# Optimization experiments

Hardware: AMD Instinct MI355X
Metric: run time of the kernel (lower is better)

The kernel has to match this reference:

```python
import jax, jax.numpy as jnp
import numpy as np

N = 100000
E = 1600000
IN_CH, HID_CH, OUT_CH = 128, 64, 32


def setup_inputs() -> dict:
    key = jax.random.key(0)
    ks = jax.random.split(key, 6)
    x = jax.random.normal(ks[0], (N, IN_CH), dtype=jnp.float32)
    ei = jax.random.randint(ks[1], (2, E), 0, N, dtype=jnp.int64)
    W1 = jax.random.normal(ks[2], (IN_CH, HID_CH), dtype=jnp.float32) * 0.05
    b1 = jax.random.normal(ks[3], (HID_CH,), dtype=jnp.float32) * 0.05
    W2 = jax.random.normal(ks[4], (HID_CH, OUT_CH), dtype=jnp.float32) * 0.05
    b2 = jax.random.normal(ks[5], (OUT_CH,), dtype=jnp.float32) * 0.05
    return {"x": x, "ei": ei, "W1": W1, "b1": b1, "W2": W2, "b2": b2}


def gcn_layer(x, sa, da, n):
    # degree with self-loops already appended in sa/da
    deg = jax.ops.segment_sum(jnp.ones((sa.shape[0],), x.dtype), da, num_segments=n)
    prod = deg[sa] * deg[da]
    norm = jnp.where(prod > 0, jax.lax.rsqrt(prod), 0.0)  # (deg_s*deg_d)^-0.5, inf->0
    msg = x[sa] * norm[:, None]            # [E+N, C] gather + scale
    return jax.ops.segment_sum(msg, da, num_segments=n)  # scatter_add


def reference(x, ei, W1, b1, W2, b2):
    n = x.shape[0]
    loop = jnp.arange(n, dtype=ei.dtype)
    sa = jnp.concatenate([ei[0], loop])
    da = jnp.concatenate([ei[1], loop])
    h = gcn_layer(x @ W1 + b1, sa, da, n)
    h = jax.nn.relu(h)
    # dropout: eval mode (training=False) -> identity
    return gcn_layer(h @ W2 + b2, sa, da, n)
```

## Files before the change

### kernel.cpp

```cpp
#include <hip/hip_runtime.h>

#define NN 100000
#define NE 1600000
#define IN_CH 128
#define HID_CH 64
#define OUT_CH 32
#define NBUCK 391
#define CHUNKA 8192

typedef unsigned short ushort_t;
typedef _Float16 half2_t __attribute__((ext_vector_type(2)));

__device__ inline ushort_t f2bf(float f) {
    union { float f; unsigned u; } v; v.f = f;
    unsigned r = v.u + 0x7fff + ((v.u >> 16) & 1);
    return (ushort_t)(r >> 16);
}
__device__ inline float blo(unsigned u) {
    union { unsigned x; float f; } v; v.x = u << 16; return v.f;
}
__device__ inline float bhi(unsigned u) {
    union { unsigned x; float f; } v; v.x = u & 0xffff0000u; return v.f;
}
__device__ inline unsigned pkh(float a, float b) {
    union { half2_t h; unsigned u; } v;
    v.h[0] = (_Float16)a; v.h[1] = (_Float16)b;
    return v.u;
}
__device__ inline half2_t u2h(unsigned u) {
    union { unsigned u; half2_t h; } v; v.u = u; return v.h;
}
__device__ inline float fdot2(unsigned a, unsigned b, float c) {
#if __has_builtin(__builtin_amdgcn_fdot2)
    return __builtin_amdgcn_fdot2(u2h(a), u2h(b), c, false);
#else
    half2_t ha = u2h(a), hb = u2h(b);
    return c + (float)ha[0] * (float)hb[0] + (float)ha[1] * (float)hb[1];
#endif
}

__global__ __launch_bounds__(256) void k_bhist(const int* __restrict__ da,
                                               int* __restrict__ bcnt) {
    __shared__ int hist[NBUCK];
    int t = threadIdx.x;
    for (int i = t; i < NBUCK; i += 256) hist[i] = 0;
    __syncthreads();
    int base = blockIdx.x * CHUNKA;
    for (int i = 0; i < CHUNKA; i += 256) {
        int e = base + i + t;
        if (e < NE) atomicAdd(&hist[da[e] >> 8], 1);
    }
    __syncthreads();
    for (int i = t; i < NBUCK; i += 256) {
        int c = hist[i];
        if (c) atomicAdd(&bcnt[i], c);
    }
}

__global__ __launch_bounds__(512) void k_bscan(const int* __restrict__ bcnt,
                                               int* __restrict__ bbase,
                                               int* __restrict__ bcur,
                                               int* __restrict__ rowptr) {
    __shared__ int lds[512];
    int t = threadIdx.x;
    int v = (t < NBUCK) ? bcnt[t] : 0;
    lds[t] = v;
    __syncthreads();
    for (int off = 1; off < 512; off <<= 1) {
        int x = (t >= off) ? lds[t - off] : 0;
        __syncthreads();
        lds[t] += x;
        __syncthreads();
    }
    int excl = lds[t] - v;
    if (t < NBUCK) { bbase[t] = excl; bcur[t] = excl; }
    if (t == 0) { bbase[NBUCK] = NE; rowptr[NN] = NE; }
}

__global__ __launch_bounds__(256) void k_bfill(const int* __restrict__ sa,
                                               const int* __restrict__ da,
                                               int* __restrict__ bcur,
                                               unsigned* __restrict__ ebuf) {
    __shared__ int hist[NBUCK];
    __shared__ int lcur[NBUCK];
    int t = threadIdx.x;
    for (int i = t; i < NBUCK; i += 256) hist[i] = 0;
    __syncthreads();
    int base = blockIdx.x * CHUNKA;
    for (int i = 0; i < CHUNKA; i += 256) {
        int e = base + i + t;
        if (e < NE) atomicAdd(&hist[da[e] >> 8], 1);
    }
    __syncthreads();
    for (int b = t; b < NBUCK; b += 256) {
        int c = hist[b];
        lcur[b] = c ? atomicAdd(&bcur[b], c) : 0;
    }
    __syncthreads();
    for (int i = 0; i < CHUNKA; i += 256) {
        int e = base + i + t;
        if (e < NE) {
            int d = da[e];
            int p = atomicAdd(&lcur[d >> 8], 1);
            ebuf[p] = ((unsigned)sa[e] << 8) | (unsigned)(d & 255);
        }
    }
}

__global__ __launch_bounds__(256) void k_bfine(const unsigned* __restrict__ ebuf,
                                               const int* __restrict__ bbase,
                                               int* __restrict__ rowptr,
                                               float* __restrict__ rs,
                                               int* __restrict__ col) {
    __shared__ int cnt[256];
    __shared__ int cur[256];
    __shared__ int scn[256];
    int b = blockIdx.x, t = threadIdx.x;
    int nb = NN - b * 256; if (nb > 256) nb = 256;
    int beg = bbase[b], end = bbase[b + 1];
    cnt[t] = 0;
    __syncthreads();
    for (int i = beg + t; i < end; i += 256) atomicAdd(&cnt[ebuf[i] & 255], 1);
    __syncthreads();
    int v = cnt[t];
    scn[t] = v;
    __syncthreads();
    for (int off = 1; off < 256; off <<= 1) {
        int x = (t >= off) ? scn[t - off] : 0;
        __syncthreads();
        scn[t] += x;
        __syncthreads();
    }
    int excl = scn[t] - v;
    if (t < nb) {
        rowptr[b * 256 + t] = beg + excl;
        rs[b * 256 + t] = rsqrtf((float)(v + 1));
        cur[t] = beg + excl;
    }
    __syncthreads();
    for (int i = beg + t; i < end; i += 256) {
        unsigned p = ebuf[i];
        int pos = atomicAdd(&cur[p & 255], 1);
        col[pos] = (int)(p >> 8);
    }
}

#define SWZU1(n, k2) ((n) * 64 + ((k2) ^ ((((n) & 7)) << 2)))
#define SWZ2(n, k) ((n) * 64 + ((k) ^ ((((n) & 7)) << 2)))

__global__ __launch_bounds__(256, 4) void k_gemm1(
    const float* __restrict__ x, const float* __restrict__ W1,
    const float* __restrict__ b1, const float* __restrict__ rs,
    ushort_t* __restrict__ xsb) {
    __shared__ unsigned xth[64 * 64];
    __shared__ unsigned w1h[64 * 64];
    int t = threadIdx.x;
    int base = blockIdx.x * 64;

#pragma unroll
    for (int i = 0; i < 8; ++i) {
        int flat = i * 1024 + t * 4;
        int node = flat >> 7, k0 = flat & 127;
        int gn = base + node;
        float4 v = make_float4(0.f, 0.f, 0.f, 0.f);
        if (gn < NN) v = *(const float4*)(x + (size_t)gn * IN_CH + k0);
        uint2 pk;
        pk.x = pkh(v.x, v.y);
        pk.y = pkh(v.z, v.w);
        *(uint2*)&xth[SWZU1(node, k0 >> 1)] = pk;
    }
#pragma unroll
    for (int i = 0; i < 16; ++i) {
        int idx = i * 256 + t;
        int k2 = idx >> 6, c = idx & 63;
        float f0 = W1[(2 * k2) * 64 + c];
        float f1 = W1[(2 * k2 + 1) * 64 + c];
        w1h[idx] = pkh(f0, f1);
    }
    __syncthreads();

    int tn = t & 15, tc = t >> 4;
    int c0 = tc * 4;
    float acc[4][4];
#pragma unroll
    for (int a = 0; a < 4; ++a)
#pragma unroll
        for (int b = 0; b < 4; ++b) acc[a][b] = 0.f;

    for (int k2 = 0; k2 < 64; k2 += 2) {
        uint2 xu[4];
#pragma unroll
        for (int jn = 0; jn < 4; ++jn)
            xu[jn] = *(uint2*)&xth[SWZU1(tn + jn * 16, k2)];
        uint4 w0 = *(uint4*)&w1h[(k2 + 0) * 64 + c0];
        uint4 w1 = *(uint4*)&w1h[(k2 + 1) * 64 + c0];
        unsigned wq0[4] = {w0.x, w0.y, w0.z, w0.w};
        unsigned wq1[4] = {w1.x, w1.y, w1.z, w1.w};
#pragma unroll
        for (int jn = 0; jn < 4; ++jn)
#pragma unroll
            for (int jc = 0; jc < 4; ++jc) {
                acc[jn][jc] = fdot2(xu[jn].x, wq0[jc], acc[jn][jc]);
                acc[jn][jc] = fdot2(xu[jn].y, wq1[jc], acc[jn][jc]);
            }
    }

    float4 bb = *(const float4*)&b1[c0];
#pragma unroll
    for (int jn = 0; jn < 4; ++jn) {
        int gn = base + tn + jn * 16;
        if (gn < NN) {
            float r = rs[gn];
            uint2 pk;
            pk.x = (unsigned)f2bf((acc[jn][0] + bb.x) * r) |
                   ((unsigned)f2bf((acc[jn][1] + bb.y) * r) << 16);
            pk.y = (unsigned)f2bf((acc[jn][2] + bb.z) * r) |
                   ((unsigned)f2bf((acc[jn][3] + bb.w) * r) << 16);
            *(uint2*)&xsb[(size_t)gn * HID_CH + c0] = pk;
        }
    }
}

__global__ __launch_bounds__(256) void k_agg1(
    const int* __restrict__ rowptr, const int* __restrict__ col,
    const ushort_t* __restrict__ xsb, const float* __restrict__ rs,
    ushort_t* __restrict__ hb) {
    int gid = blockIdx.x * blockDim.x + threadIdx.x;
    int n = gid >> 6;
    if (n >= NN) return;
    int lane = threadIdx.x & 63;
    int g = lane >> 4;
    unsigned c0 = (unsigned)(lane & 15) * 4;
    int beg = rowptr[n], end = rowptr[n + 1];

    float a0 = 0.f, a1 = 0.f, a2 = 0.f, a3 = 0.f;
    if (g == 0) {
        uint2 sv = *(const uint2*)&xsb[(unsigned)n * 64u + c0];
        a0 = blo(sv.x); a1 = bhi(sv.x); a2 = blo(sv.y); a3 = bhi(sv.y);
    }

    int i = beg;
    for (; i + 16 <= end; i += 16) {
        int s0 = col[i + g];
        int s1 = col[i + 4 + g];
        int s2 = col[i + 8 + g];
        int s3 = col[i + 12 + g];
        uint2 v0 = *(const uint2*)&xsb[(unsigned)s0 * 64u + c0];
        uint2 v1 = *(const uint2*)&xsb[(unsigned)s1 * 64u + c0];
        uint2 v2 = *(const uint2*)&xsb[(unsigned)s2 * 64u + c0];
        uint2 v3 = *(const uint2*)&xsb[(unsigned)s3 * 64u + c0];
        a0 += blo(v0.x); a1 += bhi(v0.x); a2 += blo(v0.y); a3 += bhi(v0.y);
        a0 += blo(v1.x); a1 += bhi(v1.x); a2 += blo(v1.y); a3 += bhi(v1.y);
        a0 += blo(v2.x); a1 += bhi(v2.x); a2 += blo(v2.y); a3 += bhi(v2.y);
        a0 += blo(v3.x); a1 += bhi(v3.x); a2 += blo(v3.y); a3 += bhi(v3.y);
    }
    for (; i + 4 <= end; i += 4) {
        int s0 = col[i + g];
        uint2 v0 = *(const uint2*)&xsb[(unsigned)s0 * 64u + c0];
        a0 += blo(v0.x); a1 += bhi(v0.x); a2 += blo(v0.y); a3 += bhi(v0.y);
    }
    int r = end - i;
    if (g < r) {
        int s0 = col[i + g];
        uint2 v0 = *(const uint2*)&xsb[(unsigned)s0 * 64u + c0];
        a0 += blo(v0.x); a1 += bhi(v0.x); a2 += blo(v0.y); a3 += bhi(v0.y);
    }

    a0 += __shfl_xor(a0, 16); a1 += __shfl_xor(a1, 16);
    a2 += __shfl_xor(a2, 16); a3 += __shfl_xor(a3, 16);
    a0 += __shfl_xor(a0, 32); a1 += __shfl_xor(a1, 32);
    a2 += __shfl_xor(a2, 32); a3 += __shfl_xor(a3, 32);

    if (g == 0) {
        float rn = rs[n];
        uint2 pk;
        pk.x = (unsigned)f2bf(fmaxf(a0 * rn, 0.f)) |
               ((unsigned)f2bf(fmaxf(a1 * rn, 0.f)) << 16);
        pk.y = (unsigned)f2bf(fmaxf(a2 * rn, 0.f)) |
               ((unsigned)f2bf(fmaxf(a3 * rn, 0.f)) << 16);
        *(uint2*)&hb[(unsigned)n * 64u + c0] = pk;
    }
}

__global__ __launch_bounds__(256) void k_gemm2(
    const ushort_t* __restrict__ hb, const float* __restrict__ W2,
    const float* __restrict__ b2, const float* __restrict__ rs,
    ushort_t* __restrict__ ysb) {
    __shared__ float ht[64 * 64];
    __shared__ float w2s[64 * 32];
    int t = threadIdx.x;
    int base = blockIdx.x * 64;

#pragma unroll
    for (int i = 0; i < 8; ++i) {
        int uidx = i * 256 + t;
        int node = uidx >> 5, k2 = uidx & 31;
        int gn = base + node;
        unsigned u = 0;
        if (gn < NN) u = *(const unsigned*)&hb[(size_t)gn * HID_CH + k2 * 2];
        float2 f; f.x = blo(u); f.y = bhi(u);
        *(float2*)&ht[SWZ2(node, k2 * 2)] = f;
    }
#pragma unroll
    for (int i = 0; i < 2; ++i) {
        int flat = i * 1024 + t * 4;
        *(float4*)&w2s[flat] = *(const float4*)(W2 + flat);
    }
    __syncthreads();

    int tn = t & 15, tc = t >> 4;
    int c0 = tc * 2;
    float acc[4][2];
#pragma unroll
    for (int a = 0; a < 4; ++a) { acc[a][0] = 0.f; acc[a][1] = 0.f; }

    for (int k0 = 0; k0 < 64; k0 += 4) {
        float xq[4][4], wq[4][2];
#pragma unroll
        for (int j = 0; j < 4; ++j)
            *(float2*)&wq[j][0] = *(float2*)&w2s[(k0 + j) * 32 + c0];
#pragma unroll
        for (int jn = 0; jn < 4; ++jn)
            *(float4*)&xq[jn][0] = *(float4*)&ht[SWZ2(tn + jn * 16, k0)];
#pragma unroll
        for (int jn = 0; jn < 4; ++jn)
#pragma unroll
            for (int j = 0; j < 4; ++j) {
                acc[jn][0] = fmaf(xq[jn][j], wq[j][0], acc[jn][0]);
                acc[jn][1] = fmaf(xq[jn][j], wq[j][1], acc[jn][1]);
            }
    }

    float2 bb = *(const float2*)&b2[c0];
#pragma unroll
    for (int jn = 0; jn < 4; ++jn) {
        int gn = base + tn + jn * 16;
        if (gn < NN) {
            float r = rs[gn];
            unsigned pk = (unsigned)f2bf((acc[jn][0] + bb.x) * r) |
                          ((unsigned)f2bf((acc[jn][1] + bb.y) * r) << 16);
            *(unsigned*)&ysb[(size_t)gn * OUT_CH + c0] = pk;
        }
    }
}

__global__ __launch_bounds__(256) void k_agg2(
    const int* __restrict__ rowptr, const int* __restrict__ col,
    const ushort_t* __restrict__ ysb, const float* __restrict__ rs,
    float* __restrict__ out) {
    int gid = blockIdx.x * blockDim.x + threadIdx.x;
    int n = gid >> 6;
    if (n >= NN) return;
    int lane = threadIdx.x & 63;
    int g = lane >> 3;
    unsigned c0 = (unsigned)(lane & 7) * 4;
    int beg = rowptr[n], end = rowptr[n + 1];

    float a0 = 0.f, a1 = 0.f, a2 = 0.f, a3 = 0.f;
    if (g == 0) {
        uint2 sv = *(const uint2*)&ysb[(unsigned)n * 32u + c0];
        a0 = blo(sv.x); a1 = bhi(sv.x); a2 = blo(sv.y); a3 = bhi(sv.y);
    }

    int i = beg;
    for (; i + 16 <= end; i += 16) {
        int s0 = col[i + g];
        int s1 = col[i + 8 + g];
        uint2 v0 = *(const uint2*)&ysb[(unsigned)s0 * 32u + c0];
        uint2 v1 = *(const uint2*)&ysb[(unsigned)s1 * 32u + c0];
        a0 += blo(v0.x); a1 += bhi(v0.x); a2 += blo(v0.y); a3 += bhi(v0.y);
        a0 += blo(v1.x); a1 += bhi(v1.x); a2 += blo(v1.y); a3 += bhi(v1.y);
    }
    if (i + 8 <= end) {
        int s0 = col[i + g];
        uint2 v0 = *(const uint2*)&ysb[(unsigned)s0 * 32u + c0];
        a0 += blo(v0.x); a1 += bhi(v0.x); a2 += blo(v0.y); a3 += bhi(v0.y);
        i += 8;
    }
    int r = end - i;
    if (g < r) {
        int s0 = col[i + g];
        uint2 v0 = *(const uint2*)&ysb[(unsigned)s0 * 32u + c0];
        a0 += blo(v0.x); a1 += bhi(v0.x); a2 += blo(v0.y); a3 += bhi(v0.y);
    }

    a0 += __shfl_xor(a0, 8);  a1 += __shfl_xor(a1, 8);
    a2 += __shfl_xor(a2, 8);  a3 += __shfl_xor(a3, 8);
    a0 += __shfl_xor(a0, 16); a1 += __shfl_xor(a1, 16);
    a2 += __shfl_xor(a2, 16); a3 += __shfl_xor(a3, 16);
    a0 += __shfl_xor(a0, 32); a1 += __shfl_xor(a1, 32);
    a2 += __shfl_xor(a2, 32); a3 += __shfl_xor(a3, 32);

    if (g == 0) {
        float rn = rs[n];
        float4 o;
        o.x = a0 * rn; o.y = a1 * rn; o.z = a2 * rn; o.w = a3 * rn;
        *(float4*)&out[(size_t)n * OUT_CH + c0] = o;
    }
}

extern "C" void kernel_launch(void* const* d_in, const int* in_sizes, int n_in,
                              void* d_out, int out_size, void* d_ws, size_t ws_size,
                              hipStream_t stream) {
    const float* x  = (const float*)d_in[0];
    const int*   ei = (const int*)d_in[1];
    const float* W1 = (const float*)d_in[2];
    const float* b1 = (const float*)d_in[3];
    const float* W2 = (const float*)d_in[4];
    const float* b2 = (const float*)d_in[5];
    const int* sa = ei;
    const int* da = ei + NE;

    char* ws = (char*)d_ws;
    size_t off = 0;
    auto alloc = [&](size_t bytes) {
        void* p = ws + off;
        off += (bytes + 255) & ~(size_t)255;
        return p;
    };
    int*      bcnt   = (int*)alloc((size_t)NBUCK * 4);
    int*      bbase  = (int*)alloc((size_t)(NBUCK + 1) * 4);
    int*      bcur   = (int*)alloc((size_t)NBUCK * 4);
    int*      rowptr = (int*)alloc((size_t)(NN + 1) * 4);
    float*    rs     = (float*)alloc((size_t)NN * 4);
    unsigned* ebuf   = (unsigned*)alloc((size_t)NE * 4);
    int*      col    = (int*)alloc((size_t)NE * 4);
    ushort_t* xsb    = (ushort_t*)alloc((size_t)NN * HID_CH * 2);
    ushort_t* hb     = (ushort_t*)alloc((size_t)NN * HID_CH * 2);
    ushort_t* ysb    = (ushort_t*)alloc((size_t)NN * OUT_CH * 2);
    float*    outp   = (float*)d_out;

    const int B = 256;
    const int NBLKA = (NE + CHUNKA - 1) / CHUNKA;
    hipMemsetAsync(bcnt, 0, (size_t)NBUCK * 4, stream);
    k_bhist<<<NBLKA, 256, 0, stream>>>(da, bcnt);
    k_bscan<<<1, 512, 0, stream>>>(bcnt, bbase, bcur, rowptr);
    k_bfill<<<NBLKA, 256, 0, stream>>>(sa, da, bcur, ebuf);
    k_bfine<<<NBUCK, 256, 0, stream>>>(ebuf, bbase, rowptr, rs, col);

    const int NBLK_GEMM = (NN + 63) / 64;
    k_gemm1<<<NBLK_GEMM, 256, 0, stream>>>(x, W1, b1, rs, xsb);
    k_agg1<<<(NN * 64 + B - 1) / B, B, 0, stream>>>(rowptr, col, xsb, rs, hb);
    k_gemm2<<<NBLK_GEMM, 256, 0, stream>>>(hb, W2, b2, rs, ysb);
    k_agg2<<<(NN * 64 + B - 1) / B, B, 0, stream>>>(rowptr, col, ysb, rs, outp);
}
```

Measured before the change: 222.4 us.

## Split hidden features into channel slices for cache-resident layer-1 aggregation

```diff
diff --git a/kernel.cpp b/kernel.cpp
--- a/kernel.cpp
+++ b/kernel.cpp
@@ -151,7 +151,7 @@
 __global__ __launch_bounds__(256, 4) void k_gemm1(
     const float* __restrict__ x, const float* __restrict__ W1,
     const float* __restrict__ b1, const float* __restrict__ rs,
-    ushort_t* __restrict__ xsb) {
+    ushort_t* __restrict__ xst) {
     __shared__ unsigned xth[64 * 64];
     __shared__ unsigned w1h[64 * 64];
     int t = threadIdx.x;
@@ -205,6 +205,7 @@
             }
     }
 
+    int cg = c0 >> 3, co = c0 & 7;
     float4 bb = *(const float4*)&b1[c0];
 #pragma unroll
     for (int jn = 0; jn < 4; ++jn) {
@@ -216,74 +217,63 @@
                    ((unsigned)f2bf((acc[jn][1] + bb.y) * r) << 16);
             pk.y = (unsigned)f2bf((acc[jn][2] + bb.z) * r) |
                    ((unsigned)f2bf((acc[jn][3] + bb.w) * r) << 16);
-            *(uint2*)&xsb[(size_t)gn * HID_CH + c0] = pk;
+            *(uint2*)&xst[((size_t)cg * NN + gn) * 8 + co] = pk;
         }
     }
 }
 
-__global__ __launch_bounds__(256) void k_agg1(
+__global__ __launch_bounds__(256) void k_cagg1(
     const int* __restrict__ rowptr, const int* __restrict__ col,
-    const ushort_t* __restrict__ xsb, const float* __restrict__ rs,
-    ushort_t* __restrict__ hb) {
-    int gid = blockIdx.x * blockDim.x + threadIdx.x;
-    int n = gid >> 6;
+    const ushort_t* __restrict__ xst, const float* __restrict__ rs,
+    ushort_t* __restrict__ hbt) {
+    int b = blockIdx.x;
+    int cg = b & 7;
+    int n = (b >> 3) * 256 + threadIdx.x;
     if (n >= NN) return;
-    int lane = threadIdx.x & 63;
-    int g = lane >> 4;
-    unsigned c0 = (unsigned)(lane & 15) * 4;
+    const ushort_t* sl = xst + (size_t)cg * NN * 8;
     int beg = rowptr[n], end = rowptr[n + 1];
 
-    float a0 = 0.f, a1 = 0.f, a2 = 0.f, a3 = 0.f;
-    if (g == 0) {
-        uint2 sv = *(const uint2*)&xsb[(unsigned)n * 64u + c0];
-        a0 = blo(sv.x); a1 = bhi(sv.x); a2 = blo(sv.y); a3 = bhi(sv.y);
-    }
+    uint4 sv = *(const uint4*)(sl + (size_t)n * 8);
+    float a0 = blo(sv.x), a1 = bhi(sv.x), a2 = blo(sv.y), a3 = bhi(sv.y);
+    float a4 = blo(sv.z), a5 = bhi(sv.z), a6 = blo(sv.w), a7 = bhi(sv.w);
 
     int i = beg;
-    for (; i + 16 <= end; i += 16) {
-        int s0 = col[i + g];
-        int s1 = col[i + 4 + g];
-        int s2 = col[i + 8 + g];
-        int s3 = col[i + 12 + g];
-        uint2 v0 = *(const uint2*)&xsb[(unsigned)s0 * 64u + c0];
-        uint2 v1 = *(const uint2*)&xsb[(unsigned)s1 * 64u + c0];
-        uint2 v2 = *(const uint2*)&xsb[(unsigned)s2 * 64u + c0];
-        uint2 v3 = *(const uint2*)&xsb[(unsigned)s3 * 64u + c0];
+    for (; i + 4 <= end; i += 4) {
+        int s0 = col[i], s1 = col[i + 1], s2 = col[i + 2], s3 = col[i + 3];
+        uint4 v0 = *(const uint4*)(sl + (size_t)s0 * 8);
+        uint4 v1 = *(const uint4*)(sl + (size_t)s1 * 8);
+        uint4 v2 = *(const uint4*)(sl + (size_t)s2 * 8);
+        uint4 v3 = *(const uint4*)(sl + (size_t)s3 * 8);
         a0 += blo(v0.x); a1 += bhi(v0.x); a2 += blo(v0.y); a3 += bhi(v0.y);
+        a4 += blo(v0.z); a5 += bhi(v0.z); a6 += blo(v0.w); a7 += bhi(v0.w);
         a0 += blo(v1.x); a1 += bhi(v1.x); a2 += blo(v1.y); a3 += bhi(v1.y);
+        a4 += blo(v1.z); a5 += bhi(v1.z); a6 += blo(v1.w); a7 += bhi(v1.w);
         a0 += blo(v2.x); a1 += bhi(v2.x); a2 += blo(v2.y); a3 += bhi(v2.y);
+        a4 += blo(v2.z); a5 += bhi(v2.z); a6 += blo(v2.w); a7 += bhi(v2.w);
         a0 += blo(v3.x); a1 += bhi(v3.x); a2 += blo(v3.y); a3 += bhi(v3.y);
-    }
-    for (; i + 4 <= end; i += 4) {
-        int s0 = col[i + g];
-        uint2 v0 = *(const uint2*)&xsb[(unsigned)s0 * 64u + c0];
+        a4 += blo(v3.z); a5 += bhi(v3.z); a6 += blo(v3.w); a7 += bhi(v3.w);
+    }
+    for (; i < end; ++i) {
+        uint4 v0 = *(const uint4*)(sl + (size_t)col[i] * 8);
         a0 += blo(v0.x); a1 += bhi(v0.x); a2 += blo(v0.y); a3 += bhi(v0.y);
-    }
-    int r = end - i;
-    if (g < r) {
-        int s0 = col[i + g];
-        uint2 v0 = *(const uint2*)&xsb[(unsigned)s0 * 64u + c0];
-        a0 += blo(v0.x); a1 += bhi(v0.x); a2 += blo(v0.y); a3 += bhi(v0.y);
-    }
-
-    a0 += __shfl_xor(a0, 16); a1 += __shfl_xor(a1, 16);
-    a2 += __shfl_xor(a2, 16); a3 += __shfl_xor(a3, 16);
-    a0 += __shfl_xor(a0, 32); a1 += __shfl_xor(a1, 32);
-    a2 += __shfl_xor(a2, 32); a3 += __shfl_xor(a3, 32);
-
-    if (g == 0) {
-        float rn = rs[n];
-        uint2 pk;
-        pk.x = (unsigned)f2bf(fmaxf(a0 * rn, 0.f)) |
-               ((unsigned)f2bf(fmaxf(a1 * rn, 0.f)) << 16);
-        pk.y = (unsigned)f2bf(fmaxf(a2 * rn, 0.f)) |
-               ((unsigned)f2bf(fmaxf(a3 * rn, 0.f)) << 16);
-        *(uint2*)&hb[(unsigned)n * 64u + c0] = pk;
-    }
+        a4 += blo(v0.z); a5 += bhi(v0.z); a6 += blo(v0.w); a7 += bhi(v0.w);
+    }
+
+    float rn = rs[n];
+    uint4 pk;
+    pk.x = (unsigned)f2bf(fmaxf(a0 * rn, 0.f)) |
+           ((unsigned)f2bf(fmaxf(a1 * rn, 0.f)) << 16);
+    pk.y = (unsigned)f2bf(fmaxf(a2 * rn, 0.f)) |
+           ((unsigned)f2bf(fmaxf(a3 * rn, 0.f)) << 16);
+    pk.z = (unsigned)f2bf(fmaxf(a4 * rn, 0.f)) |
+           ((unsigned)f2bf(fmaxf(a5 * rn, 0.f)) << 16);
+    pk.w = (unsigned)f2bf(fmaxf(a6 * rn, 0.f)) |
+           ((unsigned)f2bf(fmaxf(a7 * rn, 0.f)) << 16);
+    *(uint4*)(hbt + ((size_t)cg * NN + n) * 8) = pk;
 }
 
 __global__ __launch_bounds__(256) void k_gemm2(
-    const ushort_t* __restrict__ hb, const float* __restrict__ W2,
+    const ushort_t* __restrict__ hbt, const float* __restrict__ W2,
     const float* __restrict__ b2, const float* __restrict__ rs,
     ushort_t* __restrict__ ysb) {
     __shared__ float ht[64 * 64];
@@ -292,14 +282,17 @@
     int base = blockIdx.x * 64;
 
 #pragma unroll
-    for (int i = 0; i < 8; ++i) {
-        int uidx = i * 256 + t;
-        int node = uidx >> 5, k2 = uidx & 31;
+    for (int k = 0; k < 2; ++k) {
+        int idx = k * 256 + t;
+        int s = idx >> 6, node = idx & 63;
         int gn = base + node;
-        unsigned u = 0;
-        if (gn < NN) u = *(const unsigned*)&hb[(size_t)gn * HID_CH + k2 * 2];
-        float2 f; f.x = blo(u); f.y = bhi(u);
-        *(float2*)&ht[SWZ2(node, k2 * 2)] = f;
+        uint4 u = make_uint4(0, 0, 0, 0);
+        if (gn < NN) u = *(const uint4*)(hbt + ((size_t)s * NN + gn) * 8);
+        float4 f0, f1;
+        f0.x = blo(u.x); f0.y = bhi(u.x); f0.z = blo(u.y); f0.w = bhi(u.y);
+        f1.x = blo(u.z); f1.y = bhi(u.z); f1.z = blo(u.w); f1.w = bhi(u.w);
+        *(float4*)&ht[SWZ2(node, s * 8)] = f0;
+        *(float4*)&ht[SWZ2(node, s * 8 + 4)] = f1;
     }
 #pragma unroll
     for (int i = 0; i < 2; ++i) {
@@ -425,8 +418,8 @@
     float*    rs     = (float*)alloc((size_t)NN * 4);
     unsigned* ebuf   = (unsigned*)alloc((size_t)NE * 4);
     int*      col    = (int*)alloc((size_t)NE * 4);
-    ushort_t* xsb    = (ushort_t*)alloc((size_t)NN * HID_CH * 2);
-    ushort_t* hb     = (ushort_t*)alloc((size_t)NN * HID_CH * 2);
+    ushort_t* xst    = (ushort_t*)alloc((size_t)NN * HID_CH * 2);
+    ushort_t* hbt    = (ushort_t*)alloc((size_t)NN * HID_CH * 2);
     ushort_t* ysb    = (ushort_t*)alloc((size_t)NN * OUT_CH * 2);
     float*    outp   = (float*)d_out;
 
@@ -439,8 +432,8 @@
     k_bfine<<<NBUCK, 256, 0, stream>>>(ebuf, bbase, rowptr, rs, col);
 
     const int NBLK_GEMM = (NN + 63) / 64;
-    k_gemm1<<<NBLK_GEMM, 256, 0, stream>>>(x, W1, b1, rs, xsb);
-    k_agg1<<<(NN * 64 + B - 1) / B, B, 0, stream>>>(rowptr, col, xsb, rs, hb);
-    k_gemm2<<<NBLK_GEMM, 256, 0, stream>>>(hb, W2, b2, rs, ysb);
+    k_gemm1<<<NBLK_GEMM, 256, 0, stream>>>(x, W1, b1, rs, xst);
+    k_cagg1<<<8 * ((NN + 255) / 256), 256, 0, stream>>>(rowptr, col, xst, rs, hbt);
+    k_gemm2<<<NBLK_GEMM, 256, 0, stream>>>(hbt, W2, b2, rs, ysb);
     k_agg2<<<(NN * 64 + B - 1) / B, B, 0, stream>>>(rowptr, col, ysb, rs, outp);
 }
```

After: 233.4 us. +4.9%, slower.

## Use coarser 1024-node buckets for CSR build and 16-byte gathers in aggregation

Applied to the files above, without the earlier changes.

```diff
diff --git a/kernel.cpp b/kernel.cpp
--- a/kernel.cpp
+++ b/kernel.cpp
@@ -5,7 +5,7 @@
 #define IN_CH 128
 #define HID_CH 64
 #define OUT_CH 32
-#define NBUCK 391
+#define NB2 98
 #define CHUNKA 8192
 
 typedef unsigned short ushort_t;
@@ -41,91 +41,91 @@
 
 __global__ __launch_bounds__(256) void k_bhist(const int* __restrict__ da,
                                                int* __restrict__ bcnt) {
-    __shared__ int hist[NBUCK];
-    int t = threadIdx.x;
-    for (int i = t; i < NBUCK; i += 256) hist[i] = 0;
+    __shared__ int hist[4][NB2];
+    int t = threadIdx.x, w = t >> 6;
+    for (int i = t; i < 4 * NB2; i += 256) ((int*)hist)[i] = 0;
     __syncthreads();
     int base = blockIdx.x * CHUNKA;
     for (int i = 0; i < CHUNKA; i += 256) {
         int e = base + i + t;
-        if (e < NE) atomicAdd(&hist[da[e] >> 8], 1);
-    }
-    __syncthreads();
-    for (int i = t; i < NBUCK; i += 256) {
-        int c = hist[i];
-        if (c) atomicAdd(&bcnt[i], c);
-    }
-}
-
-__global__ __launch_bounds__(512) void k_bscan(const int* __restrict__ bcnt,
+        if (e < NE) atomicAdd(&hist[w][da[e] >> 10], 1);
+    }
+    __syncthreads();
+    if (t < NB2) {
+        int c = hist[0][t] + hist[1][t] + hist[2][t] + hist[3][t];
+        if (c) atomicAdd(&bcnt[t], c);
+    }
+}
+
+__global__ __launch_bounds__(128) void k_bscan(const int* __restrict__ bcnt,
                                                int* __restrict__ bbase,
                                                int* __restrict__ bcur,
                                                int* __restrict__ rowptr) {
-    __shared__ int lds[512];
+    __shared__ int lds[128];
     int t = threadIdx.x;
-    int v = (t < NBUCK) ? bcnt[t] : 0;
+    int v = (t < NB2) ? bcnt[t] : 0;
     lds[t] = v;
     __syncthreads();
-    for (int off = 1; off < 512; off <<= 1) {
+    for (int off = 1; off < 128; off <<= 1) {
         int x = (t >= off) ? lds[t - off] : 0;
         __syncthreads();
         lds[t] += x;
         __syncthreads();
     }
     int excl = lds[t] - v;
-    if (t < NBUCK) { bbase[t] = excl; bcur[t] = excl; }
-    if (t == 0) { bbase[NBUCK] = NE; rowptr[NN] = NE; }
+    if (t < NB2) { bbase[t] = excl; bcur[t] = excl; }
+    if (t == 0) { bbase[NB2] = NE; rowptr[NN] = NE; }
 }
 
 __global__ __launch_bounds__(256) void k_bfill(const int* __restrict__ sa,
                                                const int* __restrict__ da,
                                                int* __restrict__ bcur,
                                                unsigned* __restrict__ ebuf) {
-    __shared__ int hist[NBUCK];
-    __shared__ int lcur[NBUCK];
-    int t = threadIdx.x;
-    for (int i = t; i < NBUCK; i += 256) hist[i] = 0;
+    __shared__ int hist[4][NB2];
+    __shared__ int lcur[NB2];
+    int t = threadIdx.x, w = t >> 6;
+    for (int i = t; i < 4 * NB2; i += 256) ((int*)hist)[i] = 0;
     __syncthreads();
     int base = blockIdx.x * CHUNKA;
     for (int i = 0; i < CHUNKA; i += 256) {
         int e = base + i + t;
-        if (e < NE) atomicAdd(&hist[da[e] >> 8], 1);
-    }
-    __syncthreads();
-    for (int b = t; b < NBUCK; b += 256) {
-        int c = hist[b];
-        lcur[b] = c ? atomicAdd(&bcur[b], c) : 0;
+        if (e < NE) atomicAdd(&hist[w][da[e] >> 10], 1);
+    }
+    __syncthreads();
+    if (t < NB2) {
+        int c = hist[0][t] + hist[1][t] + hist[2][t] + hist[3][t];
+        lcur[t] = c ? atomicAdd(&bcur[t], c) : 0;
     }
     __syncthreads();
     for (int i = 0; i < CHUNKA; i += 256) {
         int e = base + i + t;
         if (e < NE) {
             int d = da[e];
-            int p = atomicAdd(&lcur[d >> 8], 1);
-            ebuf[p] = ((unsigned)sa[e] << 8) | (unsigned)(d & 255);
+            int p = atomicAdd(&lcur[d >> 10], 1);
+            ebuf[p] = ((unsigned)sa[e] << 10) | (unsigned)(d & 1023);
         }
     }
 }
 
-__global__ __launch_bounds__(256) void k_bfine(const unsigned* __restrict__ ebuf,
-                                               const int* __restrict__ bbase,
-                                               int* __restrict__ rowptr,
-                                               float* __restrict__ rs,
-                                               int* __restrict__ col) {
-    __shared__ int cnt[256];
-    __shared__ int cur[256];
-    __shared__ int scn[256];
+__global__ __launch_bounds__(1024) void k_bfine(const unsigned* __restrict__ ebuf,
+                                                const int* __restrict__ bbase,
+                                                int* __restrict__ rowptr,
+                                                float* __restrict__ rs,
+                                                int* __restrict__ col) {
+    __shared__ int cnt[1024];
+    __shared__ int cur[1024];
+    __shared__ int scn[1024];
     int b = blockIdx.x, t = threadIdx.x;
-    int nb = NN - b * 256; if (nb > 256) nb = 256;
+    int nb = NN - b * 1024; if (nb > 1024) nb = 1024;
     int beg = bbase[b], end = bbase[b + 1];
     cnt[t] = 0;
     __syncthreads();
-    for (int i = beg + t; i < end; i += 256) atomicAdd(&cnt[ebuf[i] & 255], 1);
+    for (int i = beg + t; i < end; i += 1024) atomicAdd(&cnt[ebuf[i] & 1023], 1);
     __syncthreads();
     int v = cnt[t];
     scn[t] = v;
     __syncthreads();
-    for (int off = 1; off < 256; off <<= 1) {
+    for (int off = 1; off < 1024; off <<= 1) {
         int x = (t >= off) ? scn[t - off] : 0;
         __syncthreads();
         scn[t] += x;
@@ -133,15 +133,15 @@
     }
     int excl = scn[t] - v;
     if (t < nb) {
-        rowptr[b * 256 + t] = beg + excl;
-        rs[b * 256 + t] = rsqrtf((float)(v + 1));
+        rowptr[b * 1024 + t] = beg + excl;
+        rs[b * 1024 + t] = rsqrtf((float)(v + 1));
         cur[t] = beg + excl;
     }
     __syncthreads();
-    for (int i = beg + t; i < end; i += 256) {
+    for (int i = beg + t; i < end; i += 1024) {
         unsigned p = ebuf[i];
-        int pos = atomicAdd(&cur[p & 255], 1);
-        col[pos] = (int)(p >> 8);
+        int pos = atomicAdd(&cur[p & 1023], 1);
+        col[pos] = (int)(p >> 10);
     }
 }
 
@@ -221,6 +221,10 @@
     }
 }
 
+#define ADD8(v) do { \
+    a0 += blo((v).x); a1 += bhi((v).x); a2 += blo((v).y); a3 += bhi((v).y); \
+    a4 += blo((v).z); a5 += bhi((v).z); a6 += blo((v).w); a7 += bhi((v).w); } while (0)
+
 __global__ __launch_bounds__(256) void k_agg1(
     const int* __restrict__ rowptr, const int* __restrict__ col,
     const ushort_t* __restrict__ xsb, const float* __restrict__ rs,
@@ -229,56 +233,59 @@
     int n = gid >> 6;
     if (n >= NN) return;
     int lane = threadIdx.x & 63;
-    int g = lane >> 4;
-    unsigned c0 = (unsigned)(lane & 15) * 4;
+    int g = lane >> 3;
+    unsigned c0 = (unsigned)(lane & 7) * 8;
     int beg = rowptr[n], end = rowptr[n + 1];
 
     float a0 = 0.f, a1 = 0.f, a2 = 0.f, a3 = 0.f;
+    float a4 = 0.f, a5 = 0.f, a6 = 0.f, a7 = 0.f;
     if (g == 0) {
-        uint2 sv = *(const uint2*)&xsb[(unsigned)n * 64u + c0];
-        a0 = blo(sv.x); a1 = bhi(sv.x); a2 = blo(sv.y); a3 = bhi(sv.y);
+        uint4 sv = *(const uint4*)&xsb[(unsigned)n * 64u + c0];
+        ADD8(sv);
     }
 
     int i = beg;
     for (; i + 16 <= end; i += 16) {
         int s0 = col[i + g];
-        int s1 = col[i + 4 + g];
-        int s2 = col[i + 8 + g];
-        int s3 = col[i + 12 + g];
-        uint2 v0 = *(const uint2*)&xsb[(unsigned)s0 * 64u + c0];
-        uint2 v1 = *(const uint2*)&xsb[(unsigned)s1 * 64u + c0];
-        uint2 v2 = *(const uint2*)&xsb[(unsigned)s2 * 64u + c0];
-        uint2 v3 = *(const uint2*)&xsb[(unsigned)s3 * 64u + c0];
-        a0 += blo(v0.x); a1 += bhi(v0.x); a2 += blo(v0.y); a3 += bhi(v0.y);
-        a0 += blo(v1.x); a1 += bhi(v1.x); a2 += blo(v1.y); a3 += bhi(v1.y);
-        a0 += blo(v2.x); a1 += bhi(v2.x); a2 += blo(v2.y); a3 += bhi(v2.y);
-        a0 += blo(v3.x); a1 += bhi(v3.x); a2 += blo(v3.y); a3 += bhi(v3.y);
-    }
-    for (; i + 4 <= end; i += 4) {
+        int s1 = col[i + 8 + g];
+        uint4 v0 = *(const uint4*)&xsb[(unsigned)s0 * 64u + c0];
+        uint4 v1 = *(const uint4*)&xsb[(unsigned)s1 * 64u + c0];
+        ADD8(v0);
+        ADD8(v1);
+    }
+    if (i + 8 <= end) {
         int s0 = col[i + g];
-        uint2 v0 = *(const uint2*)&xsb[(unsigned)s0 * 64u + c0];
-        a0 += blo(v0.x); a1 += bhi(v0.x); a2 += blo(v0.y); a3 += bhi(v0.y);
+        uint4 v0 = *(const uint4*)&xsb[(unsigned)s0 * 64u + c0];
+        ADD8(v0);
+        i += 8;
     }
     int r = end - i;
     if (g < r) {
         int s0 = col[i + g];
-        uint2 v0 = *(const uint2*)&xsb[(unsigned)s0 * 64u + c0];
-        a0 += blo(v0.x); a1 += bhi(v0.x); a2 += blo(v0.y); a3 += bhi(v0.y);
-    }
-
-    a0 += __shfl_xor(a0, 16); a1 += __shfl_xor(a1, 16);
-    a2 += __shfl_xor(a2, 16); a3 += __shfl_xor(a3, 16);
-    a0 += __shfl_xor(a0, 32); a1 += __shfl_xor(a1, 32);
-    a2 += __shfl_xor(a2, 32); a3 += __shfl_xor(a3, 32);
+        uint4 v0 = *(const uint4*)&xsb[(unsigned)s0 * 64u + c0];
+        ADD8(v0);
+    }
+
+#pragma unroll
+    for (int m = 8; m <= 32; m <<= 1) {
+        a0 += __shfl_xor(a0, m); a1 += __shfl_xor(a1, m);
+        a2 += __shfl_xor(a2, m); a3 += __shfl_xor(a3, m);
+        a4 += __shfl_xor(a4, m); a5 += __shfl_xor(a5, m);
+        a6 += __shfl_xor(a6, m); a7 += __shfl_xor(a7, m);
+    }
 
     if (g == 0) {
         float rn = rs[n];
-        uint2 pk;
+        uint4 pk;
         pk.x = (unsigned)f2bf(fmaxf(a0 * rn, 0.f)) |
                ((unsigned)f2bf(fmaxf(a1 * rn, 0.f)) << 16);
         pk.y = (unsigned)f2bf(fmaxf(a2 * rn, 0.f)) |
                ((unsigned)f2bf(fmaxf(a3 * rn, 0.f)) << 16);
-        *(uint2*)&hb[(unsigned)n * 64u + c0] = pk;
+        pk.z = (unsigned)f2bf(fmaxf(a4 * rn, 0.f)) |
+               ((unsigned)f2bf(fmaxf(a5 * rn, 0.f)) << 16);
+        pk.w = (unsigned)f2bf(fmaxf(a6 * rn, 0.f)) |
+               ((unsigned)f2bf(fmaxf(a7 * rn, 0.f)) << 16);
+        *(uint4*)&hb[(unsigned)n * 64u + c0] = pk;
     }
 }
 
@@ -352,50 +359,45 @@
     int n = gid >> 6;
     if (n >= NN) return;
     int lane = threadIdx.x & 63;
-    int g = lane >> 3;
-    unsigned c0 = (unsigned)(lane & 7) * 4;
+    int g = lane >> 2;
+    unsigned c0 = (unsigned)(lane & 3) * 8;
     int beg = rowptr[n], end = rowptr[n + 1];
 
     float a0 = 0.f, a1 = 0.f, a2 = 0.f, a3 = 0.f;
+    float a4 = 0.f, a5 = 0.f, a6 = 0.f, a7 = 0.f;
     if (g == 0) {
-        uint2 sv = *(const uint2*)&ysb[(unsigned)n * 32u + c0];
-        a0 = blo(sv.x); a1 = bhi(sv.x); a2 = blo(sv.y); a3 = bhi(sv.y);
+        uint4 sv = *(const uint4*)&ysb[(unsigned)n * 32u + c0];
+        ADD8(sv);
     }
 
     int i = beg;
     for (; i + 16 <= end; i += 16) {
         int s0 = col[i + g];
-        int s1 = col[i + 8 + g];
-        uint2 v0 = *(const uint2*)&ysb[(unsigned)s0 * 32u + c0];
-        uint2 v1 = *(const uint2*)&ysb[(unsigned)s1 * 32u + c0];
-        a0 += blo(v0.x); a1 += bhi(v0.x); a2 += blo(v0.y); a3 += bhi(v0.y);
-        a0 += blo(v1.x); a1 += bhi(v1.x); a2 += blo(v1.y); a3 += bhi(v1.y);
-    }
-    if (i + 8 <= end) {
-        int s0 = col[i + g];
-        uint2 v0 = *(const uint2*)&ysb[(unsigned)s0 * 32u + c0];
-        a0 += blo(v0.x); a1 += bhi(v0.x); a2 += blo(v0.y); a3 += bhi(v0.y);
-        i += 8;
+        uint4 v0 = *(const uint4*)&ysb[(unsigned)s0 * 32u + c0];
+        ADD8(v0);
     }
     int r = end - i;
     if (g < r) {
         int s0 = col[i + g];
-        uint2 v0 = *(const uint2*)&ysb[(unsigned)s0 * 32u + c0];
-        a0 += blo(v0.x); a1 += bhi(v0.x); a2 += blo(v0.y); a3 += bhi(v0.y);
-    }
-
-    a0 += __shfl_xor(a0, 8);  a1 += __shfl_xor(a1, 8);
-    a2 += __shfl_xor(a2, 8);  a3 += __shfl_xor(a3, 8);
-    a0 += __shfl_xor(a0, 16); a1 += __shfl_xor(a1, 16);
-    a2 += __shfl_xor(a2, 16); a3 += __shfl_xor(a3, 16);
-    a0 += __shfl_xor(a0, 32); a1 += __shfl_xor(a1, 32);
-    a2 += __shfl_xor(a2, 32); a3 += __shfl_xor(a3, 32);
+        uint4 v0 = *(const uint4*)&ysb[(unsigned)s0 * 32u + c0];
+        ADD8(v0);
+    }
+
+#pragma unroll
+    for (int m = 4; m <= 32; m <<= 1) {
+        a0 += __shfl_xor(a0, m); a1 += __shfl_xor(a1, m);
+        a2 += __shfl_xor(a2, m); a3 += __shfl_xor(a3, m);
+        a4 += __shfl_xor(a4, m); a5 += __shfl_xor(a5, m);
+        a6 += __shfl_xor(a6, m); a7 += __shfl_xor(a7, m);
+    }
 
     if (g == 0) {
         float rn = rs[n];
-        float4 o;
-        o.x = a0 * rn; o.y = a1 * rn; o.z = a2 * rn; o.w = a3 * rn;
-        *(float4*)&out[(size_t)n * OUT_CH + c0] = o;
+        float4 o0, o1;
+        o0.x = a0 * rn; o0.y = a1 * rn; o0.z = a2 * rn; o0.w = a3 * rn;
+        o1.x = a4 * rn; o1.y = a5 * rn; o1.z = a6 * rn; o1.w = a7 * rn;
+        *(float4*)&out[(size_t)n * OUT_CH + c0] = o0;
+        *(float4*)&out[(size_t)n * OUT_CH + c0 + 4] = o1;
     }
 }
 
@@ -418,9 +420,9 @@
         off += (bytes + 255) & ~(size_t)255;
         return p;
     };
-    int*      bcnt   = (int*)alloc((size_t)NBUCK * 4);
-    int*      bbase  = (int*)alloc((size_t)(NBUCK + 1) * 4);
-    int*      bcur   = (int*)alloc((size_t)NBUCK * 4);
+    int*      bcnt   = (int*)alloc((size_t)NB2 * 4);
+    int*      bbase  = (int*)alloc((size_t)(NB2 + 1) * 4);
+    int*      bcur   = (int*)alloc((size_t)NB2 * 4);
     int*      rowptr = (int*)alloc((size_t)(NN + 1) * 4);
     float*    rs     = (float*)alloc((size_t)NN * 4);
     unsigned* ebuf   = (unsigned*)alloc((size_t)NE * 4);
@@ -432,11 +434,11 @@
 
     const int B = 256;
     const int NBLKA = (NE + CHUNKA - 1) / CHUNKA;
-    hipMemsetAsync(bcnt, 0, (size_t)NBUCK * 4, stream);
+    hipMemsetAsync(bcnt, 0, (size_t)NB2 * 4, stream);
     k_bhist<<<NBLKA, 256, 0, stream>>>(da, bcnt);
-    k_bscan<<<1, 512, 0, stream>>>(bcnt, bbase, bcur, rowptr);
+    k_bscan<<<1, 128, 0, stream>>>(bcnt, bbase, bcur, rowptr);
     k_bfill<<<NBLKA, 256, 0, stream>>>(sa, da, bcur, ebuf);
-    k_bfine<<<NBUCK, 256, 0, stream>>>(ebuf, bbase, rowptr, rs, col);
+    k_bfine<<<NB2, 1024, 0, stream>>>(ebuf, bbase, rowptr, rs, col);
 
     const int NBLK_GEMM = (NN + 63) / 64;
     k_gemm1<<<NBLK_GEMM, 256, 0, stream>>>(x, W1, b1, rs, xsb);
```

Measured after the change: 222.4 us. About the same (-0.0%).
